# Performance work log

Hardware: AMD Instinct MI355X
Metric: run time of the kernel (lower is better)

## Reference

```python
import jax, jax.numpy as jnp
import numpy as np

B, D = 500000, 128
UNITS, STACK, NPRED = 4, 12, 2
EPS = 1e-3  # Keras BatchNormalization default epsilon


def setup_inputs() -> dict:
    key = jax.random.key(0)
    ks = jax.random.split(key, 2 * STACK + 4)
    inp = {"x": jax.random.normal(ks[0], (B, D), dtype=jnp.float32)}
    # 12 dense weights with growing input width D + 4*i
    for i in range(STACK):
        inp[f"w{i}"] = jax.random.normal(ks[1 + i], (D + UNITS * i, UNITS), dtype=jnp.float32) * 0.1
    inp["gamma"] = 1.0 + 0.1 * jax.random.normal(ks[STACK + 1], (STACK, UNITS), dtype=jnp.float32)
    inp["beta"] = 0.1 * jax.random.normal(ks[STACK + 2], (STACK, UNITS), dtype=jnp.float32)
    inp["mean"] = 0.1 * jax.random.normal(ks[STACK + 3], (STACK, UNITS), dtype=jnp.float32)
    inp["var"] = 0.5 + jax.random.uniform(ks[2 * STACK], (STACK, UNITS), dtype=jnp.float32)
    inp["wf"] = jax.random.normal(ks[2 * STACK + 1], (D + UNITS * STACK, NPRED), dtype=jnp.float32) * 0.1
    inp["bf"] = jnp.zeros((NPRED,), dtype=jnp.float32)
    return inp


def reference(x, w0, w1, w2, w3, w4, w5, w6, w7, w8, w9, w10, w11,
              gamma, beta, mean, var, wf, bf):
    ws = [w0, w1, w2, w3, w4, w5, w6, w7, w8, w9, w10, w11]
    h = x
    for i in range(STACK):
        y = h @ ws[i]  # [B, 4]
        # inference-mode BatchNorm, fused scale/shift
        scale = gamma[i] * jax.lax.rsqrt(var[i] + EPS)
        y = jax.nn.relu(y * scale + (beta[i] - mean[i] * scale))
        h = jnp.concatenate([y, h], axis=-1)  # width grows by 4
    logits = h @ wf + bf  # [B, 2]
    return jax.nn.softmax(logits, axis=-1)
```

## Files before the change

kernel.cpp:

```cpp
#include <hip/hip_runtime.h>

#define NROWS 500000
#define DD 128
#define NSTACK 12
#define BNEPS 1e-3f
#define NCOL 50
#define TRS 50

typedef float  v2f    __attribute__((ext_vector_type(2)));
typedef float  v4f    __attribute__((ext_vector_type(4)));
typedef float  f32x4  __attribute__((ext_vector_type(4)));
typedef __bf16 bf16x8 __attribute__((ext_vector_type(8)));

__device__ __forceinline__ unsigned short f2bf_rn(float f) {
    unsigned u = __float_as_uint(f);
    return (unsigned short)((u + 0x7FFFu + ((u >> 16) & 1u)) >> 16);
}

__global__ __launch_bounds__(256, 2) void predict_kernel(
    const float* __restrict__ x,
    const float* __restrict__ w0,  const float* __restrict__ w1,
    const float* __restrict__ w2,  const float* __restrict__ w3,
    const float* __restrict__ w4,  const float* __restrict__ w5,
    const float* __restrict__ w6,  const float* __restrict__ w7,
    const float* __restrict__ w8,  const float* __restrict__ w9,
    const float* __restrict__ w10, const float* __restrict__ w11,
    const float* __restrict__ gamma_, const float* __restrict__ beta_,
    const float* __restrict__ mean_,  const float* __restrict__ var_,
    const float* __restrict__ wf,     const float* __restrict__ bf,
    float* __restrict__ out)
{
    __shared__ __align__(16) union {
        unsigned short bsw[4][4][64][8];
        float          trow[256 * TRS];
    } sh;
    __shared__ __align__(16) float SC[48];
    __shared__ __align__(16) float SH[48];
    __shared__ float BF2[2];

    const int tid = threadIdx.x;
    const float* ws[NSTACK] = {w0,w1,w2,w3,w4,w5,w6,w7,w8,w9,w10,w11};

    for (int idx = tid; idx < 1024; idx += 256)
        ((f32x4*)&sh.bsw[0][0][0][0])[idx] = (f32x4){0.f, 0.f, 0.f, 0.f};
    __syncthreads();

#pragma unroll
    for (int i = 0; i < NSTACK; ++i) {
        const float* wsi = ws[i];
        for (int e = tid; e < 512; e += 256) {
            const int k = e >> 2, u = e & 3;
            const int n = 4 * i + u;
            const int kt = k >> 5, q = (k >> 3) & 3, j = k & 7;
            const int nt = n >> 4, lane = q * 16 + (n & 15);
            sh.bsw[kt][nt][lane][j] = f2bf_rn(wsi[16 * i + e]);
        }
    }
    {
        const int e = tid;
        const int k = e >> 1, u = e & 1;
        const int n = 48 + u;
        const int kt = k >> 5, q = (k >> 3) & 3, j = k & 7;
        const int lane = q * 16 + (n & 15);
        sh.bsw[kt][3][lane][j] = f2bf_rn(wf[96 + e]);
    }
    if (tid < 48) {
        const float sc = gamma_[tid] * __frsqrt_rn(var_[tid] + BNEPS);
        SC[tid] = sc;
        SH[tid] = beta_[tid] - mean_[tid] * sc;
    }
    if (tid < 2) BF2[tid] = bf[tid];
    __syncthreads();

    const int lane = tid & 63;
    const int wv   = tid >> 6;
    const int rowbase = blockIdx.x * 256 + wv * 64;
    const int m = lane & 15;
    const int q = lane >> 4;

    const float* arow[4];
#pragma unroll
    for (int mt = 0; mt < 4; ++mt) {
        int r = rowbase + mt * 16 + m;
        if (r > NROWS - 1) r = NROWS - 1;
        arow[mt] = x + (size_t)r * DD + q * 8;
    }

    f32x4 acc[4][4];
#pragma unroll
    for (int mt = 0; mt < 4; ++mt)
#pragma unroll
        for (int nt = 0; nt < 4; ++nt) acc[mt][nt] = (f32x4){0.f, 0.f, 0.f, 0.f};

#pragma unroll
    for (int kt = 0; kt < 4; ++kt) {
        bf16x8 bfrag[4];
#pragma unroll
        for (int nt = 0; nt < 4; ++nt)
            bfrag[nt] = *(const bf16x8*)&sh.bsw[kt][nt][lane][0];
#pragma unroll
        for (int mt = 0; mt < 4; ++mt) {
            const v4f a0 = *(const v4f*)(arow[mt] + kt * 32);
            const v4f a1 = *(const v4f*)(arow[mt] + kt * 32 + 4);
            union { unsigned short us[8]; bf16x8 bv; } au;
#pragma unroll
            for (int e = 0; e < 4; ++e) {
                au.us[e]     = f2bf_rn(a0[e]);
                au.us[4 + e] = f2bf_rn(a1[e]);
            }
#pragma unroll
            for (int nt = 0; nt < 4; ++nt)
                acc[mt][nt] = __builtin_amdgcn_mfma_f32_16x16x32_bf16(
                    au.bv, bfrag[nt], acc[mt][nt], 0, 0, 0);
        }
    }

    __syncthreads();

    float* tr = &sh.trow[wv * 64 * TRS];
#pragma unroll
    for (int mt = 0; mt < 4; ++mt)
#pragma unroll
        for (int nt = 0; nt < 4; ++nt) {
            const int c = nt * 16 + m;
            if (c < NCOL) {
#pragma unroll
                for (int r = 0; r < 4; ++r)
                    tr[(mt * 16 + q * 4 + r) * TRS + c] = acc[mt][nt][r];
            }
        }

    const float* myT = &sh.trow[(wv * 64 + lane) * TRS];
    float T[NCOL];
#pragma unroll
    for (int j = 0; j < NCOL / 2; ++j) {
        const v2f t = *(const v2f*)(myT + 2 * j);
        T[2 * j] = t.x; T[2 * j + 1] = t.y;
    }

    float y[NSTACK * 4];
#pragma unroll
    for (int i = 0; i < NSTACK; ++i) {
        float a0 = T[4 * i + 0], a1 = T[4 * i + 1];
        float a2 = T[4 * i + 2], a3 = T[4 * i + 3];
        const float* wsi = ws[i];
#pragma unroll
        for (int mr = 0; mr < 4 * i; ++mr) {
            const float hv = y[(i - 1 - (mr >> 2)) * 4 + (mr & 3)];
            a0 += hv * wsi[4 * mr + 0];
            a1 += hv * wsi[4 * mr + 1];
            a2 += hv * wsi[4 * mr + 2];
            a3 += hv * wsi[4 * mr + 3];
        }
        const v4f scv = *(const v4f*)&SC[4 * i];
        const v4f shv = *(const v4f*)&SH[4 * i];
        const float r0 = a0 * scv.x + shv.x;
        const float r1 = a1 * scv.y + shv.y;
        const float r2 = a2 * scv.z + shv.z;
        const float r3 = a3 * scv.w + shv.w;
        y[4 * i + 0] = r0 > 0.f ? r0 : 0.f;
        y[4 * i + 1] = r1 > 0.f ? r1 : 0.f;
        y[4 * i + 2] = r2 > 0.f ? r2 : 0.f;
        y[4 * i + 3] = r3 > 0.f ? r3 : 0.f;
    }

    float l0 = T[48] + BF2[0];
    float l1 = T[49] + BF2[1];
#pragma unroll
    for (int mr = 0; mr < 48; ++mr) {
        const float hv = y[(11 - (mr >> 2)) * 4 + (mr & 3)];
        l0 += hv * wf[2 * mr + 0];
        l1 += hv * wf[2 * mr + 1];
    }

    const float mx = fmaxf(l0, l1);
    const float e0 = __expf(l0 - mx);
    const float e1 = __expf(l1 - mx);
    const float inv = 1.0f / (e0 + e1);

    const int row = rowbase + lane;
    if (row < NROWS)
        *(v2f*)(out + (size_t)row * 2) = (v2f){e0 * inv, e1 * inv};
}

extern "C" void kernel_launch(void* const* d_in, const int* in_sizes, int n_in,
                              void* d_out, int out_size, void* d_ws, size_t ws_size,
                              hipStream_t stream) {
    const float* x   = (const float*)d_in[0];
    const float* w0  = (const float*)d_in[1];
    const float* w1  = (const float*)d_in[2];
    const float* w2  = (const float*)d_in[3];
    const float* w3  = (const float*)d_in[4];
    const float* w4  = (const float*)d_in[5];
    const float* w5  = (const float*)d_in[6];
    const float* w6  = (const float*)d_in[7];
    const float* w7  = (const float*)d_in[8];
    const float* w8  = (const float*)d_in[9];
    const float* w9  = (const float*)d_in[10];
    const float* w10 = (const float*)d_in[11];
    const float* w11 = (const float*)d_in[12];
    const float* gm  = (const float*)d_in[13];
    const float* bt  = (const float*)d_in[14];
    const float* mn  = (const float*)d_in[15];
    const float* vr  = (const float*)d_in[16];
    const float* wf  = (const float*)d_in[17];
    const float* bf  = (const float*)d_in[18];
    float* out = (float*)d_out;

    dim3 block(256);
    dim3 grid((NROWS + 255) / 256);
    hipLaunchKernelGGL(predict_kernel, grid, block, 0, stream,
                       x, w0, w1, w2, w3, w4, w5, w6, w7, w8, w9, w10, w11,
                       gm, bt, mn, vr, wf, bf, out);
}
```

Before: 419.2 us.

## Split fused kernel into MFMA GEMM kernel and per-row recurrence kernel

Splits the single fused kernel in two. The first kernel runs the bf16 MFMA GEMM over x, double-buffers the global loads of x across k-steps, and writes a column-major 50-column intermediate per 64-row tile to workspace. The second kernel reads that intermediate with one thread per row and runs the small stacked recurrence plus softmax. The BN scale/shift is now computed per thread from global memory instead of shared memory. This drops the large LDS transpose buffer so the GEMM kernel can run more blocks per CU. In exchange it adds a second launch and a round trip of about 100MB through global memory for the intermediate.

```diff
diff --git a/kernel.cpp b/kernel.cpp
--- a/kernel.cpp
+++ b/kernel.cpp
@@ -5,7 +5,7 @@
 #define NSTACK 12
 #define BNEPS 1e-3f
 #define NCOL 50
-#define TRS 50
+#define NTILES ((NROWS + 63) / 64)
 
 typedef float  v2f    __attribute__((ext_vector_type(2)));
 typedef float  v4f    __attribute__((ext_vector_type(4)));
@@ -17,8 +17,118 @@
     return (unsigned short)((u + 0x7FFFu + ((u >> 16) & 1u)) >> 16);
 }
 
-__global__ __launch_bounds__(256, 2) void predict_kernel(
+__global__ __launch_bounds__(256, 3) void gemm_kernel(
     const float* __restrict__ x,
+    const float* __restrict__ w0,  const float* __restrict__ w1,
+    const float* __restrict__ w2,  const float* __restrict__ w3,
+    const float* __restrict__ w4,  const float* __restrict__ w5,
+    const float* __restrict__ w6,  const float* __restrict__ w7,
+    const float* __restrict__ w8,  const float* __restrict__ w9,
+    const float* __restrict__ w10, const float* __restrict__ w11,
+    const float* __restrict__ wf,
+    float* __restrict__ T)
+{
+    __shared__ __align__(16) unsigned short bsw[4][4][64][8];
+
+    const int tid = threadIdx.x;
+    const float* ws[NSTACK] = {w0,w1,w2,w3,w4,w5,w6,w7,w8,w9,w10,w11};
+
+    for (int idx = tid; idx < 1024; idx += 256)
+        ((f32x4*)&bsw[0][0][0][0])[idx] = (f32x4){0.f, 0.f, 0.f, 0.f};
+    __syncthreads();
+
+#pragma unroll
+    for (int i = 0; i < NSTACK; ++i) {
+        const float* wsi = ws[i];
+        for (int e = tid; e < 512; e += 256) {
+            const int k = e >> 2, u = e & 3;
+            const int n = 4 * i + u;
+            const int kt = k >> 5, q = (k >> 3) & 3, j = k & 7;
+            const int nt = n >> 4, lane = q * 16 + (n & 15);
+            bsw[kt][nt][lane][j] = f2bf_rn(wsi[16 * i + e]);
+        }
+    }
+    {
+        const int e = tid;
+        const int k = e >> 1, u = e & 1;
+        const int n = 48 + u;
+        const int kt = k >> 5, q = (k >> 3) & 3, j = k & 7;
+        const int lane = q * 16 + (n & 15);
+        bsw[kt][3][lane][j] = f2bf_rn(wf[96 + e]);
+    }
+    __syncthreads();
+
+    const int lane = tid & 63;
+    const int wv   = tid >> 6;
+    const int tile = blockIdx.x * 4 + wv;
+    const int rowbase = tile * 64;
+    const int m = lane & 15;
+    const int q = lane >> 4;
+
+    const float* arow[4];
+#pragma unroll
+    for (int mt = 0; mt < 4; ++mt) {
+        int r = rowbase + mt * 16 + m;
+        if (r > NROWS - 1) r = NROWS - 1;
+        arow[mt] = x + (size_t)r * DD + q * 8;
+    }
+
+    f32x4 acc[4][4];
+#pragma unroll
+    for (int mt = 0; mt < 4; ++mt)
+#pragma unroll
+        for (int nt = 0; nt < 4; ++nt) acc[mt][nt] = (f32x4){0.f, 0.f, 0.f, 0.f};
+
+    v4f A0[2][4], A1[2][4];
+#pragma unroll
+    for (int mt = 0; mt < 4; ++mt) {
+        A0[0][mt] = *(const v4f*)(arow[mt]);
+        A1[0][mt] = *(const v4f*)(arow[mt] + 4);
+    }
+
+#pragma unroll
+    for (int kt = 0; kt < 4; ++kt) {
+        const int cur = kt & 1, nxt = cur ^ 1;
+        if (kt < 3) {
+#pragma unroll
+            for (int mt = 0; mt < 4; ++mt) {
+                A0[nxt][mt] = *(const v4f*)(arow[mt] + (kt + 1) * 32);
+                A1[nxt][mt] = *(const v4f*)(arow[mt] + (kt + 1) * 32 + 4);
+            }
+        }
+        bf16x8 bfrag[4];
+#pragma unroll
+        for (int nt = 0; nt < 4; ++nt)
+            bfrag[nt] = *(const bf16x8*)&bsw[kt][nt][lane][0];
+#pragma unroll
+        for (int mt = 0; mt < 4; ++mt) {
+            union { unsigned short us[8]; bf16x8 bv; } au;
+#pragma unroll
+            for (int e = 0; e < 4; ++e) {
+                au.us[e]     = f2bf_rn(A0[cur][mt][e]);
+                au.us[4 + e] = f2bf_rn(A1[cur][mt][e]);
+            }
+#pragma unroll
+            for (int nt = 0; nt < 4; ++nt)
+                acc[mt][nt] = __builtin_amdgcn_mfma_f32_16x16x32_bf16(
+                    au.bv, bfrag[nt], acc[mt][nt], 0, 0, 0);
+        }
+    }
+
+    float* tb = T + (size_t)tile * 4096;
+#pragma unroll
+    for (int nt = 0; nt < 4; ++nt) {
+        const int c = nt * 16 + m;
+        if (c < NCOL) {
+#pragma unroll
+            for (int mt = 0; mt < 4; ++mt)
+                *(v4f*)(tb + c * 64 + mt * 16 + q * 4) = acc[mt][nt];
+        }
+    }
+}
+
+__global__ __launch_bounds__(256, 4) void recur_kernel(
+    const float* __restrict__ T,
     const float* __restrict__ w0,  const float* __restrict__ w1,
     const float* __restrict__ w2,  const float* __restrict__ w3,
     const float* __restrict__ w4,  const float* __restrict__ w5,
@@ -30,119 +140,23 @@
     const float* __restrict__ wf,     const float* __restrict__ bf,
     float* __restrict__ out)
 {
-    __shared__ __align__(16) union {
-        unsigned short bsw[4][4][64][8];
-        float          trow[256 * TRS];
-    } sh;
-    __shared__ __align__(16) float SC[48];
-    __shared__ __align__(16) float SH[48];
-    __shared__ float BF2[2];
-
-    const int tid = threadIdx.x;
+    const int row = blockIdx.x * blockDim.x + threadIdx.x;
+    if (row >= NROWS) return;
+
     const float* ws[NSTACK] = {w0,w1,w2,w3,w4,w5,w6,w7,w8,w9,w10,w11};
 
-    for (int idx = tid; idx < 1024; idx += 256)
-        ((f32x4*)&sh.bsw[0][0][0][0])[idx] = (f32x4){0.f, 0.f, 0.f, 0.f};
-    __syncthreads();
-
+    const int tile = row >> 6, rr = row & 63;
+    const float* tb = T + (size_t)tile * 4096 + rr;
+
+    float Tv[NCOL];
+#pragma unroll
+    for (int c = 0; c < NCOL; ++c) Tv[c] = tb[c * 64];
+
+    float y[NSTACK * 4];
 #pragma unroll
     for (int i = 0; i < NSTACK; ++i) {
-        const float* wsi = ws[i];
-        for (int e = tid; e < 512; e += 256) {
-            const int k = e >> 2, u = e & 3;
-            const int n = 4 * i + u;
-            const int kt = k >> 5, q = (k >> 3) & 3, j = k & 7;
-            const int nt = n >> 4, lane = q * 16 + (n & 15);
-            sh.bsw[kt][nt][lane][j] = f2bf_rn(wsi[16 * i + e]);
-        }
-    }
-    {
-        const int e = tid;
-        const int k = e >> 1, u = e & 1;
-        const int n = 48 + u;
-        const int kt = k >> 5, q = (k >> 3) & 3, j = k & 7;
-        const int lane = q * 16 + (n & 15);
-        sh.bsw[kt][3][lane][j] = f2bf_rn(wf[96 + e]);
-    }
-    if (tid < 48) {
-        const float sc = gamma_[tid] * __frsqrt_rn(var_[tid] + BNEPS);
-        SC[tid] = sc;
-        SH[tid] = beta_[tid] - mean_[tid] * sc;
-    }
-    if (tid < 2) BF2[tid] = bf[tid];
-    __syncthreads();
-
-    const int lane = tid & 63;
-    const int wv   = tid >> 6;
-    const int rowbase = blockIdx.x * 256 + wv * 64;
-    const int m = lane & 15;
-    const int q = lane >> 4;
-
-    const float* arow[4];
-#pragma unroll
-    for (int mt = 0; mt < 4; ++mt) {
-        int r = rowbase + mt * 16 + m;
-        if (r > NROWS - 1) r = NROWS - 1;
-        arow[mt] = x + (size_t)r * DD + q * 8;
-    }
-
-    f32x4 acc[4][4];
-#pragma unroll
-    for (int mt = 0; mt < 4; ++mt)
-#pragma unroll
-        for (int nt = 0; nt < 4; ++nt) acc[mt][nt] = (f32x4){0.f, 0.f, 0.f, 0.f};
-
-#pragma unroll
-    for (int kt = 0; kt < 4; ++kt) {
-        bf16x8 bfrag[4];
-#pragma unroll
-        for (int nt = 0; nt < 4; ++nt)
-            bfrag[nt] = *(const bf16x8*)&sh.bsw[kt][nt][lane][0];
-#pragma unroll
-        for (int mt = 0; mt < 4; ++mt) {
-            const v4f a0 = *(const v4f*)(arow[mt] + kt * 32);
-            const v4f a1 = *(const v4f*)(arow[mt] + kt * 32 + 4);
-            union { unsigned short us[8]; bf16x8 bv; } au;
-#pragma unroll
-            for (int e = 0; e < 4; ++e) {
-                au.us[e]     = f2bf_rn(a0[e]);
-                au.us[4 + e] = f2bf_rn(a1[e]);
-            }
-#pragma unroll
-            for (int nt = 0; nt < 4; ++nt)
-                acc[mt][nt] = __builtin_amdgcn_mfma_f32_16x16x32_bf16(
-                    au.bv, bfrag[nt], acc[mt][nt], 0, 0, 0);
-        }
-    }
-
-    __syncthreads();
-
-    float* tr = &sh.trow[wv * 64 * TRS];
-#pragma unroll
-    for (int mt = 0; mt < 4; ++mt)
-#pragma unroll
-        for (int nt = 0; nt < 4; ++nt) {
-            const int c = nt * 16 + m;
-            if (c < NCOL) {
-#pragma unroll
-                for (int r = 0; r < 4; ++r)
-                    tr[(mt * 16 + q * 4 + r) * TRS + c] = acc[mt][nt][r];
-            }
-        }
-
-    const float* myT = &sh.trow[(wv * 64 + lane) * TRS];
-    float T[NCOL];
-#pragma unroll
-    for (int j = 0; j < NCOL / 2; ++j) {
-        const v2f t = *(const v2f*)(myT + 2 * j);
-        T[2 * j] = t.x; T[2 * j + 1] = t.y;
-    }
-
-    float y[NSTACK * 4];
-#pragma unroll
-    for (int i = 0; i < NSTACK; ++i) {
-        float a0 = T[4 * i + 0], a1 = T[4 * i + 1];
-        float a2 = T[4 * i + 2], a3 = T[4 * i + 3];
+        float a0 = Tv[4 * i + 0], a1 = Tv[4 * i + 1];
+        float a2 = Tv[4 * i + 2], a3 = Tv[4 * i + 3];
         const float* wsi = ws[i];
 #pragma unroll
         for (int mr = 0; mr < 4 * i; ++mr) {
@@ -152,20 +166,18 @@
             a2 += hv * wsi[4 * mr + 2];
             a3 += hv * wsi[4 * mr + 3];
         }
-        const v4f scv = *(const v4f*)&SC[4 * i];
-        const v4f shv = *(const v4f*)&SH[4 * i];
-        const float r0 = a0 * scv.x + shv.x;
-        const float r1 = a1 * scv.y + shv.y;
-        const float r2 = a2 * scv.z + shv.z;
-        const float r3 = a3 * scv.w + shv.w;
-        y[4 * i + 0] = r0 > 0.f ? r0 : 0.f;
-        y[4 * i + 1] = r1 > 0.f ? r1 : 0.f;
-        y[4 * i + 2] = r2 > 0.f ? r2 : 0.f;
-        y[4 * i + 3] = r3 > 0.f ? r3 : 0.f;
-    }
-
-    float l0 = T[48] + BF2[0];
-    float l1 = T[49] + BF2[1];
+#pragma unroll
+        for (int u = 0; u < 4; ++u) {
+            const float sc = gamma_[4 * i + u] * __frsqrt_rn(var_[4 * i + u] + BNEPS);
+            const float sh = beta_[4 * i + u] - mean_[4 * i + u] * sc;
+            const float a  = (u == 0 ? a0 : u == 1 ? a1 : u == 2 ? a2 : a3);
+            const float v  = a * sc + sh;
+            y[4 * i + u] = v > 0.f ? v : 0.f;
+        }
+    }
+
+    float l0 = Tv[48] + bf[0];
+    float l1 = Tv[49] + bf[1];
 #pragma unroll
     for (int mr = 0; mr < 48; ++mr) {
         const float hv = y[(11 - (mr >> 2)) * 4 + (mr & 3)];
@@ -177,10 +189,7 @@
     const float e0 = __expf(l0 - mx);
     const float e1 = __expf(l1 - mx);
     const float inv = 1.0f / (e0 + e1);
-
-    const int row = rowbase + lane;
-    if (row < NROWS)
-        *(v2f*)(out + (size_t)row * 2) = (v2f){e0 * inv, e1 * inv};
+    *(v2f*)(out + (size_t)row * 2) = (v2f){e0 * inv, e1 * inv};
 }
 
 extern "C" void kernel_launch(void* const* d_in, const int* in_sizes, int n_in,
@@ -206,10 +215,20 @@
     const float* wf  = (const float*)d_in[17];
     const float* bf  = (const float*)d_in[18];
     float* out = (float*)d_out;
-
-    dim3 block(256);
-    dim3 grid((NROWS + 255) / 256);
-    hipLaunchKernelGGL(predict_kernel, grid, block, 0, stream,
-                       x, w0, w1, w2, w3, w4, w5, w6, w7, w8, w9, w10, w11,
-                       gm, bt, mn, vr, wf, bf, out);
-}
+    float* T   = (float*)d_ws;
+
+    {
+        dim3 block(256);
+        dim3 grid((NTILES + 3) / 4);
+        hipLaunchKernelGGL(gemm_kernel, grid, block, 0, stream,
+                           x, w0, w1, w2, w3, w4, w5, w6, w7, w8, w9, w10, w11,
+                           wf, T);
+    }
+    {
+        dim3 block(256);
+        dim3 grid((NROWS + 255) / 256);
+        hipLaunchKernelGGL(recur_kernel, grid, block, 0, stream,
+                           T, w0, w1, w2, w3, w4, w5, w6, w7, w8, w9, w10, w11,
+                           gm, bt, mn, vr, wf, bf, out);
+    }
+}
```

Measured after the change: 447.6 us. 1.07x slower.
